# Kernel optimization log

Measured on AMD Instinct MI355X. Metric: run time of the kernel, lower is better.

Reference implementation:

```python
import jax, jax.numpy as jnp
import numpy as np

V = 100000
E = 800000
D = 128
K = 8
EDGE_FEAT = 16
VEH_FEAT_DIM = 8
N_VEH = 16
N_LAYERS = 2
LN_EPS = 1e-5


def _ln(x, g, b):
    m = jnp.mean(x, axis=-1, keepdims=True)
    v = jnp.mean(jnp.square(x - m), axis=-1, keepdims=True)
    return (x - m) * jax.lax.rsqrt(v + LN_EPS) * g + b


def setup_inputs() -> dict:
    key = jax.random.key(0)
    ks = jax.random.split(key, 12)
    s = lambda fan_in: 1.0 / np.sqrt(fan_in)
    return {
        "Z_node_full": jax.random.normal(ks[0], (V, D), jnp.float32),
        "visit_meta": jax.random.uniform(ks[1], (V, 1 + K + 1), jnp.float32),
        "veh_feat": jax.random.normal(ks[2], (N_VEH, VEH_FEAT_DIM), jnp.float32),
        "edge_attr": jax.random.normal(ks[3], (E, EDGE_FEAT), jnp.float32),
        "edge_src": jax.random.randint(ks[4], (E,), 0, V, jnp.int32),
        "edge_dst": jax.random.randint(ks[5], (E,), 0, V, jnp.int32),
        "current_nodes": jax.random.randint(ks[6], (N_VEH,), 0, V, jnp.int32),
        "node_proj_w": jax.random.normal(ks[7], (D + 1 + K + 1, D), jnp.float32) * s(D + 1 + K + 1),
        "node_proj_b": jnp.zeros((D,), jnp.float32),
        "layers_w1": jax.random.normal(ks[8], (N_LAYERS, D + EDGE_FEAT, D), jnp.float32) * s(D + EDGE_FEAT),
        "layers_b1": jnp.zeros((N_LAYERS, D), jnp.float32),
        "layers_w2": jax.random.normal(ks[9], (N_LAYERS, D, D), jnp.float32) * s(D),
        "layers_b2": jnp.zeros((N_LAYERS, D), jnp.float32),
        "layers_ln_g": jnp.ones((N_LAYERS, D), jnp.float32),
        "layers_ln_b": jnp.zeros((N_LAYERS, D), jnp.float32),
        "props_w1": jax.random.normal(ks[10], (VEH_FEAT_DIM, D), jnp.float32) * s(VEH_FEAT_DIM),
        "props_b1": jnp.zeros((D,), jnp.float32),
        "props_w2": jax.random.normal(ks[11], (D, D), jnp.float32) * s(D),
        "props_b2": jnp.zeros((D,), jnp.float32),
        "ro_g": jnp.ones((D,), jnp.float32),
        "ro_b": jnp.zeros((D,), jnp.float32),
    }


def reference(Z_node_full, visit_meta, veh_feat, edge_attr, edge_src, edge_dst,
              current_nodes, node_proj_w, node_proj_b, layers_w1, layers_b1,
              layers_w2, layers_b2, layers_ln_g, layers_ln_b, props_w1, props_b1,
              props_w2, props_b2, ro_g, ro_b):
    # node projection: [V, D+K+2] @ [D+K+2, D]
    h_in = jnp.concatenate([Z_node_full, visit_meta], axis=-1)
    h = h_in @ node_proj_w + node_proj_b

    # per-receiver edge count, clamped to 1 (shared across layers)
    count = jax.ops.segment_sum(jnp.ones((edge_dst.shape[0],), h.dtype), edge_dst,
                                num_segments=h.shape[0])
    count = jnp.maximum(count, 1.0)[:, None]  # [V, 1]

    for l in range(N_LAYERS):
        h_src = h[edge_src]                                   # [E, D] gather
        x = jnp.concatenate([h_src, edge_attr], axis=-1)      # [E, D+edge_feat]
        msg = jax.nn.relu(x @ layers_w1[l] + layers_b1[l]) @ layers_w2[l] + layers_b2[l]
        agg = jax.ops.segment_sum(msg, edge_dst, num_segments=h.shape[0]) / count
        h = _ln(h + agg, layers_ln_g[l], layers_ln_b[l])

    props = jax.nn.relu(veh_feat @ props_w1 + props_b1) @ props_w2 + props_b2
    Z_veh = h[current_nodes]                                  # [N_veh, D] readout gather
    return _ln(Z_veh + props, ro_g, ro_b)
```

## Files before the change

### kernel.cpp

```cpp
#include <hip/hip_runtime.h>
#include <hip/hip_bf16.h>

#define V_N 100000
#define VP  100096
#define E_N 800000
#define NVEH 16
#define LN_EPS 1e-5f
#define NTILES (VP / 64)

typedef unsigned int uint;
typedef unsigned short ushort;
typedef unsigned char uchar;
typedef __attribute__((ext_vector_type(8))) short bf8_t;
typedef __attribute__((ext_vector_type(4))) float f4_t;

__device__ __forceinline__ float bf2f(ushort u) {
    union { uint i; float f; } c; c.i = ((uint)u) << 16; return c.f;
}
__device__ __forceinline__ ushort f2bf(float f) {
    union { float f; uint i; } c; c.f = f; uint x = c.i;
    return (ushort)((x + 0x7FFFu + ((x >> 16) & 1u)) >> 16);
}
__device__ __forceinline__ uint pk2(float a, float b) {
    return (uint)f2bf(a) | ((uint)f2bf(b) << 16);
}

__global__ __launch_bounds__(256) void k_pack(const float* __restrict__ W, uint4* __restrict__ dst,
                                              int nslots, int krows) {
    int slot = blockIdx.x * 256 + threadIdx.x;
    if (slot >= nslots) return;
    int ks = slot >> 9;
    int ct = (slot >> 6) & 7;
    int l  = slot & 63;
    int k0 = ks * 32 + ((l >> 4) << 3);
    int col = (ct << 4) + (l & 15);
    ushort u[8];
#pragma unroll
    for (int e = 0; e < 8; ++e) {
        int k = k0 + e;
        u[e] = (k < krows) ? f2bf(W[(size_t)k * 128 + col]) : (ushort)0;
    }
    uint4 p;
    p.x = (uint)u[0] | ((uint)u[1] << 16);
    p.y = (uint)u[2] | ((uint)u[3] << 16);
    p.z = (uint)u[4] | ((uint)u[5] << 16);
    p.w = (uint)u[6] | ((uint)u[7] << 16);
    dst[slot] = p;
}

__global__ __launch_bounds__(256) void k_count(const int* __restrict__ dst, int* __restrict__ cnt) {
    int i = blockIdx.x * blockDim.x + threadIdx.x;
    if (i < E_N) atomicAdd(&cnt[dst[i]], 1);
}

__global__ __launch_bounds__(256) void k_scan1(const int* __restrict__ cnt, int* __restrict__ rowptr,
                                               int* __restrict__ part) {
    __shared__ int sh[256];
    const int tid = threadIdx.x;
    const int base = blockIdx.x * 1024 + tid * 4;
    int v0 = (base + 0 < V_N) ? cnt[base + 0] : 0;
    int v1 = (base + 1 < V_N) ? cnt[base + 1] : 0;
    int v2 = (base + 2 < V_N) ? cnt[base + 2] : 0;
    int v3 = (base + 3 < V_N) ? cnt[base + 3] : 0;
    int s = v0 + v1 + v2 + v3;
    sh[tid] = s; __syncthreads();
    for (int off = 1; off < 256; off <<= 1) {
        int t = (tid >= off) ? sh[tid - off] : 0;
        __syncthreads();
        sh[tid] += t;
        __syncthreads();
    }
    int excl = sh[tid] - s;
    if (tid == 255) part[blockIdx.x] = sh[255];
    int run = excl;
    if (base + 0 < V_N) rowptr[base + 0] = run; run += v0;
    if (base + 1 < V_N) rowptr[base + 1] = run; run += v1;
    if (base + 2 < V_N) rowptr[base + 2] = run; run += v2;
    if (base + 3 < V_N) rowptr[base + 3] = run;
}

__global__ __launch_bounds__(128) void k_scan2(const int* __restrict__ part, int* __restrict__ pex, int nb) {
    __shared__ int sh[128];
    const int tid = threadIdx.x;
    int v = (tid < nb) ? part[tid] : 0;
    sh[tid] = v; __syncthreads();
    for (int off = 1; off < 128; off <<= 1) {
        int t = (tid >= off) ? sh[tid - off] : 0;
        __syncthreads();
        sh[tid] += t;
        __syncthreads();
    }
    if (tid < nb) pex[tid] = sh[tid] - v;
}

__global__ __launch_bounds__(256) void k_scan3(int* __restrict__ rowptr, const int* __restrict__ pex,
                                               int* __restrict__ cursor) {
    int i = blockIdx.x * 256 + threadIdx.x;
    if (i < V_N) {
        int rp = rowptr[i] + pex[i >> 10];
        rowptr[i] = rp;
        cursor[i] = rp;
    }
    if (i == 0) rowptr[V_N] = E_N;
}

__global__ __launch_bounds__(256) void k_scatter(const int* __restrict__ src, const int* __restrict__ dst,
                                                 int* __restrict__ cursor, int2* __restrict__ pes) {
    int e = blockIdx.x * 256 + threadIdx.x;
    if (e < E_N) {
        int d = dst[e];
        int p = atomicAdd(&cursor[d], 1);
        pes[p] = make_int2(e, src[e]);
    }
}

__global__ __launch_bounds__(256) void k_nodeproj(const float* __restrict__ Z, const float* __restrict__ meta,
                                                  const uint4* __restrict__ Bpk, const float* __restrict__ b,
                                                  ushort* __restrict__ hb) {
    __shared__ uint4 Bs4[2560];
    const int tid = threadIdx.x;
    for (int slot = tid; slot < 2560; slot += 256) Bs4[slot] = Bpk[slot];
    __syncthreads();
    const int lane = tid & 63, wid = tid >> 6;
    const int l15 = lane & 15, l4 = lane >> 4;
    float bcol[8];
#pragma unroll
    for (int ct = 0; ct < 8; ++ct) bcol[ct] = b[ct * 16 + l15];
    const int tile = blockIdx.x;
    int rowA = tile * 64 + wid * 16 + l15;
    int rowAc = rowA < V_N ? rowA : V_N - 1;
    const float* zp = Z + (size_t)rowAc * 128;
    union { uint4 u; bf8_t b; } afr[5];
#pragma unroll
    for (int ks = 0; ks < 4; ++ks) {
        int k0 = ks * 32 + l4 * 8;
        float4 f0 = *(const float4*)(zp + k0);
        float4 f1 = *(const float4*)(zp + k0 + 4);
        afr[ks].u.x = pk2(f0.x, f0.y);
        afr[ks].u.y = pk2(f0.z, f0.w);
        afr[ks].u.z = pk2(f1.x, f1.y);
        afr[ks].u.w = pk2(f1.z, f1.w);
    }
    {
        const float* mp = meta + (size_t)rowAc * 10;
        int f0 = l4 * 8;
        ushort u[8];
#pragma unroll
        for (int e = 0; e < 8; ++e) {
            int f = f0 + e;
            u[e] = (f < 10) ? f2bf(mp[f]) : (ushort)0;
        }
        afr[4].u.x = (uint)u[0] | ((uint)u[1] << 16);
        afr[4].u.y = (uint)u[2] | ((uint)u[3] << 16);
        afr[4].u.z = (uint)u[4] | ((uint)u[5] << 16);
        afr[4].u.w = (uint)u[6] | ((uint)u[7] << 16);
    }
    f4_t acc[8];
#pragma unroll
    for (int ct = 0; ct < 8; ++ct) acc[ct] = (f4_t){bcol[ct], bcol[ct], bcol[ct], bcol[ct]};
#pragma unroll
    for (int ks = 0; ks < 5; ++ks) {
#pragma unroll
        for (int ct = 0; ct < 8; ++ct) {
            union { uint4 u; bf8_t b; } cb; cb.u = Bs4[(ks * 8 + ct) * 64 + lane];
            acc[ct] = __builtin_amdgcn_mfma_f32_16x16x32_bf16(afr[ks].b, cb.b, acc[ct], 0, 0, 0);
        }
    }
    const int rowC0 = tile * 64 + wid * 16 + l4 * 4;
#pragma unroll
    for (int ct = 0; ct < 8; ++ct) {
        int col = ct * 16 + l15;
#pragma unroll
        for (int r = 0; r < 4; ++r) {
            int row = rowC0 + r;
            if (row < V_N) hb[(size_t)row * 128 + col] = f2bf(acc[ct][r]);
        }
    }
}

__global__ __launch_bounds__(256) void k_gemm1(const ushort* __restrict__ hb, const uint4* __restrict__ Bpk,
                                               const float* __restrict__ b, ushort* __restrict__ tb) {
    __shared__ uint4 Bs4[2048];
    const int tid = threadIdx.x;
    for (int slot = tid; slot < 2048; slot += 256) Bs4[slot] = Bpk[slot];
    __syncthreads();
    const int lane = tid & 63, wid = tid >> 6;
    const int l15 = lane & 15, l4 = lane >> 4;
    float bcol[8];
#pragma unroll
    for (int ct = 0; ct < 8; ++ct) bcol[ct] = b[ct * 16 + l15];
    const int tile = blockIdx.x;
    const int rowA = tile * 64 + wid * 16 + l15;
    const uint4* ap = (const uint4*)(hb + (size_t)rowA * 128);
    f4_t acc[8];
#pragma unroll
    for (int ct = 0; ct < 8; ++ct) acc[ct] = (f4_t){bcol[ct], bcol[ct], bcol[ct], bcol[ct]};
#pragma unroll
    for (int ks = 0; ks < 4; ++ks) {
        union { uint4 u; bf8_t b; } ca; ca.u = ap[ks * 4 + l4];
#pragma unroll
        for (int ct = 0; ct < 8; ++ct) {
            union { uint4 u; bf8_t b; } cb; cb.u = Bs4[(ks * 8 + ct) * 64 + lane];
            acc[ct] = __builtin_amdgcn_mfma_f32_16x16x32_bf16(ca.b, cb.b, acc[ct], 0, 0, 0);
        }
    }
    const int rowC0 = tile * 64 + wid * 16 + l4 * 4;
#pragma unroll
    for (int ct = 0; ct < 8; ++ct) {
        int col = ct * 16 + l15;
#pragma unroll
        for (int r = 0; r < 4; ++r) {
            int row = rowC0 + r;
            if (row < V_N) tb[(size_t)row * 128 + col] = f2bf(acc[ct][r]);
        }
    }
}

__global__ __launch_bounds__(256) void k_edge_mlp(const float* __restrict__ ea,
                                                  const int2* __restrict__ pes,
                                                  const uint4* __restrict__ Bpk,
                                                  uchar* __restrict__ U) {
    __shared__ uint4 Bs4[512];
    const int tid = threadIdx.x;
    for (int slot = tid; slot < 512; slot += 256) Bs4[slot] = Bpk[slot];
    __syncthreads();
    const int lane = tid & 63, wid = tid >> 6;
    const int l15 = lane & 15, l4 = lane >> 4;
    const long ebase = (long)blockIdx.x * 64 + wid * 16;
    union { uint4 u; bf8_t b; } afr;
    afr.u = make_uint4(0u, 0u, 0u, 0u);
    if (l4 < 2) {
        int eidx = pes[ebase + l15].x;
        const float* ep = ea + (size_t)eidx * 16 + l4 * 8;
        float4 f0 = *(const float4*)ep;
        float4 f1 = *(const float4*)(ep + 4);
        afr.u.x = pk2(f0.x, f0.y);
        afr.u.y = pk2(f0.z, f0.w);
        afr.u.z = pk2(f1.x, f1.y);
        afr.u.w = pk2(f1.z, f1.w);
    }
    f4_t acc[8];
#pragma unroll
    for (int ct = 0; ct < 8; ++ct) acc[ct] = (f4_t){0.f, 0.f, 0.f, 0.f};
#pragma unroll
    for (int ct = 0; ct < 8; ++ct) {
        union { uint4 u; bf8_t b; } cb; cb.u = Bs4[ct * 64 + lane];
        acc[ct] = __builtin_amdgcn_mfma_f32_16x16x32_bf16(afr.b, cb.b, acc[ct], 0, 0, 0);
    }
    const long rowC0 = ebase + l4 * 4;
#pragma unroll
    for (int ct = 0; ct < 8; ++ct) {
        int col = ct * 16 + l15;
#pragma unroll
        for (int r = 0; r < 4; ++r) {
            int pk = __builtin_amdgcn_cvt_pk_fp8_f32(acc[ct][r], acc[ct][r], 0, false);
            U[(size_t)(rowC0 + r) * 128 + col] = (uchar)(pk & 0xff);
        }
    }
}

__global__ __launch_bounds__(256) void k_edge_agg2(const ushort* __restrict__ tb,
                                                   const uchar* __restrict__ U,
                                                   const int2* __restrict__ pes,
                                                   const int* __restrict__ rowptr,
                                                   ushort* __restrict__ S) {
    const int lane = threadIdx.x & 63;
    const int wid  = threadIdx.x >> 6;
    const int v = blockIdx.x * 4 + wid;
    if (v >= V_N) return;
    const int st = rowptr[v], en = rowptr[v + 1];
    const int co = 2 * lane;
    float a0 = 0.f, a1 = 0.f;
    for (int i0 = st; i0 < en; i0 += 8) {
        const int n = en - i0;
        int idx[8];
#pragma unroll
        for (int j = 0; j < 8; ++j) idx[j] = (j < n) ? (i0 + j) : i0;
        int s[8];
#pragma unroll
        for (int j = 0; j < 8; ++j) s[j] = pes[idx[j]].y;
        uint tv[8]; ushort uv[8];
#pragma unroll
        for (int j = 0; j < 8; ++j) {
            tv[j] = *(const uint*)(tb + (size_t)s[j] * 128 + co);
            uv[j] = *(const ushort*)(U + (size_t)idx[j] * 128 + co);
        }
#pragma unroll
        for (int j = 0; j < 8; ++j) {
            auto uf = __builtin_amdgcn_cvt_pk_f32_fp8((int)uv[j], false);
            float p0 = bf2f((ushort)(tv[j] & 0xffffu)) + uf[0];
            float p1 = bf2f((ushort)(tv[j] >> 16)) + uf[1];
            if (j < n) { a0 += fmaxf(p0, 0.f); a1 += fmaxf(p1, 0.f); }
        }
    }
    int dg = en - st;
    float inv = 1.f / (float)(dg > 1 ? dg : 1);
    *(uint*)(S + (size_t)v * 128 + co) = pk2(a0 * inv, a1 * inv);
}

__global__ __launch_bounds__(256) void k_node_update(const ushort* __restrict__ S, ushort* __restrict__ hb,
                                                     const int* __restrict__ cnt,
                                                     const uint4* __restrict__ Bpk, const float* __restrict__ b2,
                                                     const float* __restrict__ g, const float* __restrict__ bt) {
    __shared__ uint4 Bs4[2048];
    const int tid = threadIdx.x;
    for (int slot = tid; slot < 2048; slot += 256) Bs4[slot] = Bpk[slot];
    __syncthreads();
    const int lane = tid & 63, wid = tid >> 6;
    const int l15 = lane & 15, l4 = lane >> 4;
    float b2c[8], gc[8], btc[8];
#pragma unroll
    for (int ct = 0; ct < 8; ++ct) {
        int col = ct * 16 + l15;
        b2c[ct] = b2[col]; gc[ct] = g[col]; btc[ct] = bt[col];
    }
    const int tile = blockIdx.x;
    const int rowA = tile * 64 + wid * 16 + l15;
    const uint4* ap = (const uint4*)(S + (size_t)rowA * 128);
    f4_t acc[8];
#pragma unroll
    for (int ct = 0; ct < 8; ++ct) acc[ct] = (f4_t){0.f, 0.f, 0.f, 0.f};
#pragma unroll
    for (int ks = 0; ks < 4; ++ks) {
        union { uint4 u; bf8_t b; } ca; ca.u = ap[ks * 4 + l4];
#pragma unroll
        for (int ct = 0; ct < 8; ++ct) {
            union { uint4 u; bf8_t b; } cb; cb.u = Bs4[(ks * 8 + ct) * 64 + lane];
            acc[ct] = __builtin_amdgcn_mfma_f32_16x16x32_bf16(ca.b, cb.b, acc[ct], 0, 0, 0);
        }
    }
    const int rowC0 = tile * 64 + wid * 16 + l4 * 4;
    float mask[4];
#pragma unroll
    for (int r = 0; r < 4; ++r) {
        int row = rowC0 + r;
        int dg = (row < V_N) ? cnt[row] : 0;
        mask[r] = (dg > 0) ? 1.f : 0.f;
    }
    float x[8][4];
#pragma unroll
    for (int ct = 0; ct < 8; ++ct) {
        int col = ct * 16 + l15;
#pragma unroll
        for (int r = 0; r < 4; ++r) {
            float hv = bf2f(hb[(size_t)(rowC0 + r) * 128 + col]);
            x[ct][r] = hv + acc[ct][r] + b2c[ct] * mask[r];
        }
    }
#pragma unroll
    for (int r = 0; r < 4; ++r) {
        float s = 0.f;
#pragma unroll
        for (int ct = 0; ct < 8; ++ct) s += x[ct][r];
        s += __shfl_xor(s, 1); s += __shfl_xor(s, 2);
        s += __shfl_xor(s, 4); s += __shfl_xor(s, 8);
        float mean = s * (1.f / 128.f);
        float vv = 0.f;
#pragma unroll
        for (int ct = 0; ct < 8; ++ct) { float d = x[ct][r] - mean; vv = fmaf(d, d, vv); }
        vv += __shfl_xor(vv, 1); vv += __shfl_xor(vv, 2);
        vv += __shfl_xor(vv, 4); vv += __shfl_xor(vv, 8);
        float rs = rsqrtf(vv * (1.f / 128.f) + LN_EPS);
        int row = rowC0 + r;
        bool ok = row < V_N;
#pragma unroll
        for (int ct = 0; ct < 8; ++ct) {
            int col = ct * 16 + l15;
            float y = (x[ct][r] - mean) * rs * gc[ct] + btc[ct];
            if (ok) hb[(size_t)row * 128 + col] = f2bf(y);
        }
    }
}

__global__ __launch_bounds__(128) void k_final(const ushort* __restrict__ hb, const int* __restrict__ cur,
                                               const float* __restrict__ veh,
                                               const float* __restrict__ pw1, const float* __restrict__ pb1,
                                               const float* __restrict__ pw2, const float* __restrict__ pb2,
                                               const float* __restrict__ g, const float* __restrict__ bt,
                                               float* __restrict__ out) {
    __shared__ float hid[128];
    __shared__ float red[2];
    const int i = blockIdx.x;
    const int j = threadIdx.x;
    float a = pb1[j];
#pragma unroll
    for (int f = 0; f < 8; ++f) a = fmaf(veh[i * 8 + f], pw1[f * 128 + j], a);
    hid[j] = fmaxf(a, 0.f);
    __syncthreads();
    float o = pb2[j] + bf2f(hb[(size_t)cur[i] * 128 + j]);
    for (int k = 0; k < 128; ++k) o = fmaf(hid[k], pw2[k * 128 + j], o);
    const int lane = j & 63, wid = j >> 6;
    float s = o;
#pragma unroll
    for (int off = 32; off > 0; off >>= 1) s += __shfl_xor(s, off);
    if (lane == 0) red[wid] = s;
    __syncthreads();
    float mean = (red[0] + red[1]) * (1.f / 128.f);
    __syncthreads();
    float d = o - mean;
    float vv = d * d;
#pragma unroll
    for (int off = 32; off > 0; off >>= 1) vv += __shfl_xor(vv, off);
    if (lane == 0) red[wid] = vv;
    __syncthreads();
    float var = (red[0] + red[1]) * (1.f / 128.f);
    float r = rsqrtf(var + LN_EPS);
    out[i * 128 + j] = d * r * g[j] + bt[j];
}

extern "C" void kernel_launch(void* const* d_in, const int* in_sizes, int n_in,
                              void* d_out, int out_size, void* d_ws, size_t ws_size,
                              hipStream_t stream) {
    const float* Z    = (const float*)d_in[0];
    const float* meta = (const float*)d_in[1];
    const float* veh  = (const float*)d_in[2];
    const float* ea   = (const float*)d_in[3];
    const int*   esrc = (const int*)d_in[4];
    const int*   edst = (const int*)d_in[5];
    const int*   cur  = (const int*)d_in[6];
    const float* npw  = (const float*)d_in[7];
    const float* npb  = (const float*)d_in[8];
    const float* w1   = (const float*)d_in[9];
    const float* b1   = (const float*)d_in[10];
    const float* w2   = (const float*)d_in[11];
    const float* b2   = (const float*)d_in[12];
    const float* lng  = (const float*)d_in[13];
    const float* lnb  = (const float*)d_in[14];
    const float* pw1  = (const float*)d_in[15];
    const float* pb1  = (const float*)d_in[16];
    const float* pw2  = (const float*)d_in[17];
    const float* pb2  = (const float*)d_in[18];
    const float* rog  = (const float*)d_in[19];
    const float* rob  = (const float*)d_in[20];

    ushort* hb = (ushort*)d_ws;
    ushort* tb = hb + (size_t)VP * 128;
    ushort* S  = tb + (size_t)VP * 128;
    int* cnt    = (int*)(S + (size_t)VP * 128);
    int* rowptr = cnt + VP;
    int* cursor = rowptr + VP;
    int2* pes   = (int2*)(cursor + VP);
    int* part   = (int*)(pes + E_N);
    int* pex    = part + 128;
    uint4* Bnp  = (uint4*)(pex + 128);
    uint4* Bw1b = Bnp + 2560;
    uint4* Bw1a = Bw1b + 2 * 2048;
    uint4* Bw2  = Bw1a + 2 * 512;
    uchar* U    = (uchar*)(Bw2 + 2 * 2048);
    float* out = (float*)d_out;

    const int NB = (V_N + 1023) / 1024;

    k_pack<<<10, 256, 0, stream>>>(npw, Bnp, 2560, 138);
    for (int l = 0; l < 2; ++l) {
        const float* W1b = w1 + (size_t)l * 144 * 128;
        const float* W1a = W1b + 128 * 128;
        k_pack<<<8, 256, 0, stream>>>(W1b, Bw1b + l * 2048, 2048, 128);
        k_pack<<<2, 256, 0, stream>>>(W1a, Bw1a + l * 512, 512, 16);
        k_pack<<<8, 256, 0, stream>>>(w2 + (size_t)l * 128 * 128, Bw2 + l * 2048, 2048, 128);
    }

    hipMemsetAsync(cnt, 0, VP * sizeof(int), stream);
    k_count<<<(E_N + 255) / 256, 256, 0, stream>>>(edst, cnt);
    k_scan1<<<NB, 256, 0, stream>>>(cnt, rowptr, part);
    k_scan2<<<1, 128, 0, stream>>>(part, pex, NB);
    k_scan3<<<(V_N + 255) / 256, 256, 0, stream>>>(rowptr, pex, cursor);
    k_scatter<<<(E_N + 255) / 256, 256, 0, stream>>>(esrc, edst, cursor, pes);
    k_nodeproj<<<NTILES, 256, 0, stream>>>(Z, meta, Bnp, npb, hb);

    for (int l = 0; l < 2; ++l) {
        k_gemm1<<<NTILES, 256, 0, stream>>>(hb, Bw1b + l * 2048, b1 + l * 128, tb);
        k_edge_mlp<<<E_N / 64, 256, 0, stream>>>(ea, pes, Bw1a + l * 512, U);
        k_edge_agg2<<<V_N / 4, 256, 0, stream>>>(tb, U, pes, rowptr, S);
        k_node_update<<<NTILES, 256, 0, stream>>>(S, hb, cnt, Bw2 + l * 2048,
                                                  b2 + l * 128, lng + l * 128, lnb + l * 128);
    }
    k_final<<<NVEH, 128, 0, stream>>>(hb, cur, veh, pw1, pb1, pw2, pb2, rog, rob, out);
}
```

Before: 571.7 us.

## Fuse edge MLP with segmented aggregation via shared-memory messages and atomics

Merges the edge-attribute MLP and the per-destination aggregation into one kernel. Messages stay in shared memory as fp32 instead of round-tripping through a global fp8 buffer. Each wave walks 16 dst-sorted edges and does a segmented reduction, writing fully owned segments directly and using float atomics for segments that cross chunk boundaries. The degree normalisation moves into the node-update GEMM load. This adds a per-layer memset of an fp32 accumulation buffer, a wider int4 edge record, and atomic contention on boundary rows.

```diff
diff --git a/kernel.cpp b/kernel.cpp
--- a/kernel.cpp
+++ b/kernel.cpp
@@ -7,10 +7,10 @@
 #define NVEH 16
 #define LN_EPS 1e-5f
 #define NTILES (VP / 64)
+#define MSTR 132
 
 typedef unsigned int uint;
 typedef unsigned short ushort;
-typedef unsigned char uchar;
 typedef __attribute__((ext_vector_type(8))) short bf8_t;
 typedef __attribute__((ext_vector_type(4))) float f4_t;
 
@@ -105,12 +105,12 @@
 }
 
 __global__ __launch_bounds__(256) void k_scatter(const int* __restrict__ src, const int* __restrict__ dst,
-                                                 int* __restrict__ cursor, int2* __restrict__ pes) {
+                                                 int* __restrict__ cursor, int4* __restrict__ pes4) {
     int e = blockIdx.x * 256 + threadIdx.x;
     if (e < E_N) {
         int d = dst[e];
         int p = atomicAdd(&cursor[d], 1);
-        pes[p] = make_int2(e, src[e]);
+        pes4[p] = make_int4(e, src[e], d, 0);
     }
 }
 
@@ -216,21 +216,25 @@
     }
 }
 
-__global__ __launch_bounds__(256) void k_edge_mlp(const float* __restrict__ ea,
-                                                  const int2* __restrict__ pes,
-                                                  const uint4* __restrict__ Bpk,
-                                                  uchar* __restrict__ U) {
+__global__ __launch_bounds__(256) void k_edge_fused(const float* __restrict__ ea,
+                                                    const int4* __restrict__ pes4,
+                                                    const uint4* __restrict__ Bpk,
+                                                    const ushort* __restrict__ tb,
+                                                    const int* __restrict__ rowptr,
+                                                    float* __restrict__ S) {
     __shared__ uint4 Bs4[512];
+    __shared__ float msg[64 * MSTR];
     const int tid = threadIdx.x;
     for (int slot = tid; slot < 512; slot += 256) Bs4[slot] = Bpk[slot];
     __syncthreads();
     const int lane = tid & 63, wid = tid >> 6;
     const int l15 = lane & 15, l4 = lane >> 4;
-    const long ebase = (long)blockIdx.x * 64 + wid * 16;
+    const long base = (long)blockIdx.x * 64;
+    const long ebase = base + wid * 16;
     union { uint4 u; bf8_t b; } afr;
     afr.u = make_uint4(0u, 0u, 0u, 0u);
     if (l4 < 2) {
-        int eidx = pes[ebase + l15].x;
+        int eidx = pes4[ebase + l15].x;
         const float* ep = ea + (size_t)eidx * 16 + l4 * 8;
         float4 f0 = *(const float4*)ep;
         float4 f1 = *(const float4*)(ep + 4);
@@ -247,58 +251,52 @@
         union { uint4 u; bf8_t b; } cb; cb.u = Bs4[ct * 64 + lane];
         acc[ct] = __builtin_amdgcn_mfma_f32_16x16x32_bf16(afr.b, cb.b, acc[ct], 0, 0, 0);
     }
-    const long rowC0 = ebase + l4 * 4;
+    const int lr0 = wid * 16 + l4 * 4;
 #pragma unroll
     for (int ct = 0; ct < 8; ++ct) {
         int col = ct * 16 + l15;
 #pragma unroll
-        for (int r = 0; r < 4; ++r) {
-            int pk = __builtin_amdgcn_cvt_pk_fp8_f32(acc[ct][r], acc[ct][r], 0, false);
-            U[(size_t)(rowC0 + r) * 128 + col] = (uchar)(pk & 0xff);
-        }
-    }
-}
-
-__global__ __launch_bounds__(256) void k_edge_agg2(const ushort* __restrict__ tb,
-                                                   const uchar* __restrict__ U,
-                                                   const int2* __restrict__ pes,
-                                                   const int* __restrict__ rowptr,
-                                                   ushort* __restrict__ S) {
-    const int lane = threadIdx.x & 63;
-    const int wid  = threadIdx.x >> 6;
-    const int v = blockIdx.x * 4 + wid;
-    if (v >= V_N) return;
-    const int st = rowptr[v], en = rowptr[v + 1];
+        for (int r = 0; r < 4; ++r) msg[(lr0 + r) * MSTR + col] = acc[ct][r];
+    }
+    __syncthreads();
+    const int q = wid;
     const int co = 2 * lane;
     float a0 = 0.f, a1 = 0.f;
-    for (int i0 = st; i0 < en; i0 += 8) {
-        const int n = en - i0;
-        int idx[8];
-#pragma unroll
-        for (int j = 0; j < 8; ++j) idx[j] = (j < n) ? (i0 + j) : i0;
-        int s[8];
-#pragma unroll
-        for (int j = 0; j < 8; ++j) s[j] = pes[idx[j]].y;
-        uint tv[8]; ushort uv[8];
-#pragma unroll
-        for (int j = 0; j < 8; ++j) {
-            tv[j] = *(const uint*)(tb + (size_t)s[j] * 128 + co);
-            uv[j] = *(const ushort*)(U + (size_t)idx[j] * 128 + co);
-        }
-#pragma unroll
-        for (int j = 0; j < 8; ++j) {
-            auto uf = __builtin_amdgcn_cvt_pk_f32_fp8((int)uv[j], false);
-            float p0 = bf2f((ushort)(tv[j] & 0xffffu)) + uf[0];
-            float p1 = bf2f((ushort)(tv[j] >> 16)) + uf[1];
-            if (j < n) { a0 += fmaxf(p0, 0.f); a1 += fmaxf(p1, 0.f); }
-        }
-    }
-    int dg = en - st;
-    float inv = 1.f / (float)(dg > 1 ? dg : 1);
-    *(uint*)(S + (size_t)v * 128 + co) = pk2(a0 * inv, a1 * inv);
-}
-
-__global__ __launch_bounds__(256) void k_node_update(const ushort* __restrict__ S, ushort* __restrict__ hb,
+    int ja = q * 16;
+    int vcur = pes4[base + ja].z;
+#pragma unroll 4
+    for (int j = q * 16; j < q * 16 + 16; ++j) {
+        int4 pe = pes4[base + j];
+        if (pe.z != vcur) {
+            int st = rowptr[vcur], en = rowptr[vcur + 1];
+            if (st == base + ja && en == base + j) {
+                S[(size_t)vcur * 128 + co] = a0;
+                S[(size_t)vcur * 128 + co + 1] = a1;
+            } else {
+                atomicAdd(&S[(size_t)vcur * 128 + co], a0);
+                atomicAdd(&S[(size_t)vcur * 128 + co + 1], a1);
+            }
+            vcur = pe.z; ja = j; a0 = 0.f; a1 = 0.f;
+        }
+        float2 m = *(const float2*)&msg[j * MSTR + co];
+        uint tv = *(const uint*)(tb + (size_t)pe.y * 128 + co);
+        a0 += fmaxf(bf2f((ushort)(tv & 0xffffu)) + m.x, 0.f);
+        a1 += fmaxf(bf2f((ushort)(tv >> 16)) + m.y, 0.f);
+    }
+    {
+        int jb = q * 16 + 16;
+        int st = rowptr[vcur], en = rowptr[vcur + 1];
+        if (st == base + ja && en == base + jb) {
+            S[(size_t)vcur * 128 + co] = a0;
+            S[(size_t)vcur * 128 + co + 1] = a1;
+        } else {
+            atomicAdd(&S[(size_t)vcur * 128 + co], a0);
+            atomicAdd(&S[(size_t)vcur * 128 + co + 1], a1);
+        }
+    }
+}
+
+__global__ __launch_bounds__(256) void k_node_update(const float* __restrict__ S, ushort* __restrict__ hb,
                                                      const int* __restrict__ cnt,
                                                      const uint4* __restrict__ Bpk, const float* __restrict__ b2,
                                                      const float* __restrict__ g, const float* __restrict__ bt) {
@@ -316,13 +314,25 @@
     }
     const int tile = blockIdx.x;
     const int rowA = tile * 64 + wid * 16 + l15;
-    const uint4* ap = (const uint4*)(S + (size_t)rowA * 128);
+    const int rowAc = rowA < V_N ? rowA : V_N - 1;
+    {
+    }
+    int ca_ = cnt[rowAc];
+    const float invA = 1.f / (float)(ca_ > 1 ? ca_ : 1);
+    const float* sp = S + (size_t)rowAc * 128;
     f4_t acc[8];
 #pragma unroll
     for (int ct = 0; ct < 8; ++ct) acc[ct] = (f4_t){0.f, 0.f, 0.f, 0.f};
 #pragma unroll
     for (int ks = 0; ks < 4; ++ks) {
-        union { uint4 u; bf8_t b; } ca; ca.u = ap[ks * 4 + l4];
+        int k0 = ks * 32 + l4 * 8;
+        float4 f0 = *(const float4*)(sp + k0);
+        float4 f1 = *(const float4*)(sp + k0 + 4);
+        union { uint4 u; bf8_t b; } ca;
+        ca.u.x = pk2(f0.x * invA, f0.y * invA);
+        ca.u.y = pk2(f0.z * invA, f0.w * invA);
+        ca.u.z = pk2(f1.x * invA, f1.y * invA);
+        ca.u.w = pk2(f1.z * invA, f1.w * invA);
 #pragma unroll
         for (int ct = 0; ct < 8; ++ct) {
             union { uint4 u; bf8_t b; } cb; cb.u = Bs4[(ks * 8 + ct) * 64 + lane];
@@ -435,18 +445,17 @@
 
     ushort* hb = (ushort*)d_ws;
     ushort* tb = hb + (size_t)VP * 128;
-    ushort* S  = tb + (size_t)VP * 128;
-    int* cnt    = (int*)(S + (size_t)VP * 128);
+    float*  Sf = (float*)(tb + (size_t)VP * 128);
+    int* cnt    = (int*)(Sf + (size_t)VP * 128);
     int* rowptr = cnt + VP;
     int* cursor = rowptr + VP;
-    int2* pes   = (int2*)(cursor + VP);
-    int* part   = (int*)(pes + E_N);
+    int4* pes4  = (int4*)(cursor + VP);
+    int* part   = (int*)(pes4 + E_N);
     int* pex    = part + 128;
     uint4* Bnp  = (uint4*)(pex + 128);
     uint4* Bw1b = Bnp + 2560;
     uint4* Bw1a = Bw1b + 2 * 2048;
     uint4* Bw2  = Bw1a + 2 * 512;
-    uchar* U    = (uchar*)(Bw2 + 2 * 2048);
     float* out = (float*)d_out;
 
     const int NB = (V_N + 1023) / 1024;
@@ -465,14 +474,14 @@
     k_scan1<<<NB, 256, 0, stream>>>(cnt, rowptr, part);
     k_scan2<<<1, 128, 0, stream>>>(part, pex, NB);
     k_scan3<<<(V_N + 255) / 256, 256, 0, stream>>>(rowptr, pex, cursor);
-    k_scatter<<<(E_N + 255) / 256, 256, 0, stream>>>(esrc, edst, cursor, pes);
+    k_scatter<<<(E_N + 255) / 256, 256, 0, stream>>>(esrc, edst, cursor, pes4);
     k_nodeproj<<<NTILES, 256, 0, stream>>>(Z, meta, Bnp, npb, hb);
 
     for (int l = 0; l < 2; ++l) {
         k_gemm1<<<NTILES, 256, 0, stream>>>(hb, Bw1b + l * 2048, b1 + l * 128, tb);
-        k_edge_mlp<<<E_N / 64, 256, 0, stream>>>(ea, pes, Bw1a + l * 512, U);
-        k_edge_agg2<<<V_N / 4, 256, 0, stream>>>(tb, U, pes, rowptr, S);
-        k_node_update<<<NTILES, 256, 0, stream>>>(S, hb, cnt, Bw2 + l * 2048,
+        hipMemsetAsync(Sf, 0, (size_t)V_N * 128 * sizeof(float), stream);
+        k_edge_fused<<<E_N / 64, 256, 0, stream>>>(ea, pes4, Bw1a + l * 512, tb, rowptr, Sf);
+        k_node_update<<<NTILES, 256, 0, stream>>>(Sf, hb, cnt, Bw2 + l * 2048,
                                                   b2 + l * 128, lng + l * 128, lnb + l * 128);
     }
     k_final<<<NVEH, 128, 0, stream>>>(hb, cur, veh, pw1, pb1, pw2, pb2, rog, rob, out);
```

New measurement: 767.5 us. 1.34x slower.
